# Kernel tuning notes

Hardware: AMD Instinct MI355X
Metric: run time of the kernel (lower is better)

The kernel has to match this reference:

```python
import jax, jax.numpy as jnp
import numpy as np

B, S, N_WIRES, EMBED_DIM, NUM_HEADS = 4, 2048, 8, 512, 8
D_K = EMBED_DIM // NUM_HEADS


def setup_inputs() -> dict:
    key = jax.random.key(0)
    k_x, k_th, k_q, k_k, k_v, k_c = jax.random.split(key, 6)
    x = jax.random.normal(k_x, (B, S, N_WIRES), dtype=jnp.float32)
    # trainable RX rotation angles, one per wire
    theta = jax.random.normal(k_th, (N_WIRES,), dtype=jnp.float32) * 0.1
    # nn.Linear(n_wires, embed_dim, bias=False) weights have shape (embed_dim, n_wires)
    sc_in = 1.0 / np.sqrt(N_WIRES)
    Wq = jax.random.normal(k_q, (EMBED_DIM, N_WIRES), dtype=jnp.float32) * sc_in
    Wk = jax.random.normal(k_k, (EMBED_DIM, N_WIRES), dtype=jnp.float32) * sc_in
    Wv = jax.random.normal(k_v, (EMBED_DIM, N_WIRES), dtype=jnp.float32) * sc_in
    Wc = jax.random.normal(k_c, (EMBED_DIM, EMBED_DIM), dtype=jnp.float32) * (1.0 / np.sqrt(EMBED_DIM))
    return {"x": x, "theta": theta, "Wq": Wq, "Wk": Wk, "Wv": Wv, "Wc": Wc}


def reference(x, theta, Wq, Wk, Wv, Wc):
    # Quantum encoding closed form: RX(x_i) then RX(theta_i) on |0> per wire gives <Z> = cos(x_i + theta_i).
    proj = jnp.cos(x + theta)  # (B, S, n_wires)
    b, s, _ = proj.shape
    q = jnp.einsum('bsn,en->bse', proj, Wq)
    k = jnp.einsum('bsn,en->bse', proj, Wk)
    v = jnp.einsum('bsn,en->bse', proj, Wv)
    # split heads: (B, H, S, d_k)
    q = q.reshape(b, s, NUM_HEADS, D_K).transpose(0, 2, 1, 3)
    k = k.reshape(b, s, NUM_HEADS, D_K).transpose(0, 2, 1, 3)
    v = v.reshape(b, s, NUM_HEADS, D_K).transpose(0, 2, 1, 3)
    scores = jnp.einsum('bhqd,bhkd->bhqk', q, k) / np.sqrt(D_K).astype(np.float32)
    attn = jax.nn.softmax(scores, axis=-1)  # dropout is identity at inference
    out = jnp.einsum('bhqk,bhkd->bhqd', attn, v)
    out = out.transpose(0, 2, 1, 3).reshape(b, s, EMBED_DIM)
    return jnp.einsum('bse,fe->bsf', out, Wc)
```

## Files before the change

### kernel.cpp

```cpp
#include <hip/hip_runtime.h>
#include <stdint.h>

#define N_B 4
#define S_LEN 2048
#define N_H 8
#define E_DIM 512

typedef __attribute__((ext_vector_type(8))) short bf16x8;
typedef __attribute__((ext_vector_type(4))) float f32x4;
typedef __attribute__((ext_vector_type(4))) unsigned int u32x4;
typedef __attribute__((ext_vector_type(2))) unsigned int u32x2;
typedef __attribute__((ext_vector_type(4))) unsigned short u16x4;
typedef __attribute__((ext_vector_type(8))) unsigned short u16x8;

#define MFMA16(a, b, c) __builtin_amdgcn_mfma_f32_16x16x32_bf16((a), (b), (c), 0, 0, 0)

__device__ __forceinline__ unsigned short f2bf(float f) {
    union { float f; unsigned int u; } v; v.f = f;
    unsigned int r = v.u + 0x7fffu + ((v.u >> 16) & 1u);
    return (unsigned short)(r >> 16);
}

__device__ __forceinline__ unsigned int pack2bf(float lo, float hi) {
    union { float f; unsigned int u; } a, b; a.f = lo; b.f = hi;
    return __builtin_amdgcn_perm(b.u + 0x8000u, a.u + 0x8000u, 0x07060302u);
}

__device__ __forceinline__ float fexp2(float x) {
#if __has_builtin(__builtin_amdgcn_exp2f)
    return __builtin_amdgcn_exp2f(x);
#else
    return exp2f(x);
#endif
}

#define Q_SCALE 0.18033688f

__global__ __launch_bounds__(256) void qkv_kernel(
    const float* __restrict__ x, const float* __restrict__ theta,
    const float* __restrict__ Wq, const float* __restrict__ Wk,
    const float* __restrict__ Wv,
    unsigned short* __restrict__ Q, unsigned short* __restrict__ K,
    unsigned short* __restrict__ Vt)
{
    __shared__ float proj[32][8];
    const int tid = threadIdx.x;
    const int mat = blockIdx.x % 3;
    const int chunk = blockIdx.x / 3;
    const int row0 = chunk * 32;
    const int b = row0 >> 11;
    const int s_in_b = row0 & (S_LEN - 1);

    proj[tid >> 3][tid & 7] = cosf(x[row0 * 8 + tid] + theta[tid & 7]);
    __syncthreads();

    if (mat < 2) {
        const float* W = (mat == 0) ? Wq : Wk;
        const float scale = (mat == 0) ? Q_SCALE : 1.0f;
        unsigned short* outp = (mat == 0) ? Q : K;
        const int eg = (tid & 127) * 4;
        const int sg = (tid >> 7) * 16;
        float w[4][8];
        #pragma unroll
        for (int e = 0; e < 4; ++e)
            #pragma unroll
            for (int n = 0; n < 8; ++n)
                w[e][n] = W[(eg + e) * 8 + n] * scale;
        const int h = eg >> 6, d0 = eg & 63;
        unsigned short* p0 = outp + ((size_t)(b * N_H + h) * S_LEN + s_in_b + sg) * 64 + d0;
        #pragma unroll 4
        for (int s = 0; s < 16; ++s) {
            f32x4 pa = *(const f32x4*)&proj[sg + s][0];
            f32x4 pc = *(const f32x4*)&proj[sg + s][4];
            u16x4 o;
            #pragma unroll
            for (int e = 0; e < 4; ++e) {
                float a = 0.f;
                #pragma unroll
                for (int n = 0; n < 4; ++n)
                    a += pa[n] * w[e][n] + pc[n] * w[e][n + 4];
                o[e] = f2bf(a);
            }
            *(u16x4*)&p0[s * 64] = o;
        }
    } else {
        f32x4 ps[8][2];
        const int sl0 = (tid & 3) * 8;
        #pragma unroll
        for (int k2 = 0; k2 < 8; ++k2) {
            ps[k2][0] = *(const f32x4*)&proj[sl0 + k2][0];
            ps[k2][1] = *(const f32x4*)&proj[sl0 + k2][4];
        }
        const int ecol = tid >> 2;
        for (int pass = 0; pass < 8; ++pass) {
            const int e = pass * 64 + ecol;
            const int h = e >> 6, dd = e & 63;
            float wr[8];
            #pragma unroll
            for (int n = 0; n < 8; ++n) wr[n] = Wv[e * 8 + n];
            u16x8 pk;
            #pragma unroll
            for (int k2 = 0; k2 < 8; ++k2) {
                float acc = 0.f;
                #pragma unroll
                for (int n = 0; n < 4; ++n)
                    acc += ps[k2][0][n] * wr[n] + ps[k2][1][n] * wr[n + 4];
                pk[k2] = f2bf(acc);
            }
            *(u16x8*)&Vt[((size_t)(b * N_H + h) * 64 + dd) * S_LEN + s_in_b + sl0] = pk;
        }
    }
}

__global__ __launch_bounds__(256, 4) void flash_kernel(
    const unsigned short* __restrict__ Q, const unsigned short* __restrict__ K,
    const unsigned short* __restrict__ Vt, unsigned short* __restrict__ O)
{
    __shared__ short kt[64 * 72];
    __shared__ short vt[64 * 72];
    __shared__ short pb[128 * 72];

    const int tid = threadIdx.x;
    const int lane = tid & 63, w = tid >> 6;
    const int quad = lane >> 4, lq = lane & 15;
    const int qt = blockIdx.x & 15, bh = blockIdx.x >> 4;
    const int b = bh >> 3, h = bh & 7;

    const unsigned short* Qb = Q + (size_t)bh * S_LEN * 64;
    const unsigned short* Kb = K + (size_t)bh * S_LEN * 64;
    const unsigned short* Vb = Vt + (size_t)bh * 64 * S_LEN;

    bf16x8 qf[2][2];
    #pragma unroll
    for (int mt = 0; mt < 2; ++mt)
        #pragma unroll
        for (int ks = 0; ks < 2; ++ks)
            qf[mt][ks] = *(const bf16x8*)&Qb[(size_t)(qt * 128 + w * 32 + mt * 16 + lq) * 64 + ks * 32 + quad * 8];

    f32x4 oacc[2][4];
    #pragma unroll
    for (int mt = 0; mt < 2; ++mt)
        #pragma unroll
        for (int dt = 0; dt < 4; ++dt) oacc[mt][dt] = 0.f;
    float lsum[2] = {0.f, 0.f};

    u32x4 pkr[2], pvr[2];
    #pragma unroll
    for (int i = 0; i < 2; ++i) {
        const int u = tid + (i << 8);
        pkr[i] = *(const u32x4*)&Kb[(size_t)(u >> 3) * 64 + (u & 7) * 8];
        pvr[i] = *(const u32x4*)&Vb[(size_t)(u >> 3) * S_LEN + (u & 7) * 8];
    }

    for (int kti = 0; kti < 32; ++kti) {
        __syncthreads();
        #pragma unroll
        for (int i = 0; i < 2; ++i) {
            const int u = tid + (i << 8);
            *(u32x4*)&kt[(u >> 3) * 72 + (u & 7) * 8] = pkr[i];
            *(u32x4*)&vt[(u >> 3) * 72 + (u & 7) * 8] = pvr[i];
        }
        __syncthreads();

        const int kb2 = (kti < 31) ? (kti + 1) * 64 : 0;
        #pragma unroll
        for (int i = 0; i < 2; ++i) {
            const int u = tid + (i << 8);
            pkr[i] = *(const u32x4*)&Kb[(size_t)(kb2 + (u >> 3)) * 64 + (u & 7) * 8];
            pvr[i] = *(const u32x4*)&Vb[(size_t)(u >> 3) * S_LEN + kb2 + (u & 7) * 8];
        }

        f32x4 sacc[2][4];
        #pragma unroll
        for (int mt = 0; mt < 2; ++mt)
            #pragma unroll
            for (int mts = 0; mts < 4; ++mts) sacc[mt][mts] = 0.f;
        #pragma unroll
        for (int mts = 0; mts < 4; ++mts) {
            #pragma unroll
            for (int ks = 0; ks < 2; ++ks) {
                bf16x8 af = *(const bf16x8*)&kt[(mts * 16 + lq) * 72 + ks * 32 + quad * 8];
                sacc[0][mts] = MFMA16(af, qf[0][ks], sacc[0][mts]);
                sacc[1][mts] = MFMA16(af, qf[1][ks], sacc[1][mts]);
            }
        }

        #pragma unroll
        for (int mt = 0; mt < 2; ++mt) {
            #pragma unroll
            for (int mts = 0; mts < 4; ++mts) {
                f32x4 p;
                #pragma unroll
                for (int e = 0; e < 4; ++e) p[e] = fexp2(sacc[mt][mts][e]);
                lsum[mt] += (p[0] + p[1]) + (p[2] + p[3]);
                u32x2 pw = { pack2bf(p[0], p[1]), pack2bf(p[2], p[3]) };
                *(u32x2*)&pb[(w * 32 + mt * 16 + lq) * 72 + mts * 16 + quad * 4] = pw;
            }
        }

        #pragma unroll
        for (int ks = 0; ks < 2; ++ks) {
            bf16x8 af0 = *(const bf16x8*)&pb[(w * 32 + lq) * 72 + ks * 32 + quad * 8];
            bf16x8 af1 = *(const bf16x8*)&pb[(w * 32 + 16 + lq) * 72 + ks * 32 + quad * 8];
            #pragma unroll
            for (int dt = 0; dt < 4; ++dt) {
                bf16x8 bf = *(const bf16x8*)&vt[(dt * 16 + lq) * 72 + ks * 32 + quad * 8];
                oacc[0][dt] = MFMA16(af0, bf, oacc[0][dt]);
                oacc[1][dt] = MFMA16(af1, bf, oacc[1][dt]);
            }
        }
    }

    #pragma unroll
    for (int mt = 0; mt < 2; ++mt) {
        float rs = lsum[mt];
        rs += __shfl_xor(rs, 16);
        rs += __shfl_xor(rs, 32);
        const float inv = 1.0f / rs;
        #pragma unroll
        for (int r = 0; r < 4; ++r) {
            const float ir = __shfl(inv, quad * 4 + r);
            const int row = qt * 128 + w * 32 + mt * 16 + quad * 4 + r;
            unsigned short* dst = &O[((size_t)b * S_LEN + row) * E_DIM + h * 64];
            #pragma unroll
            for (int dt = 0; dt < 4; ++dt)
                dst[dt * 16 + lq] = f2bf(oacc[mt][dt][r] * ir);
        }
    }
}

__global__ __launch_bounds__(256, 4) void outproj_kernel(
    const unsigned short* __restrict__ O, const float* __restrict__ Wc,
    float* __restrict__ Y)
{
    __shared__ short at[64 * 72];
    __shared__ short bt[64 * 72];
    const int tid = threadIdx.x;
    const int lane = tid & 63, w = tid >> 6;
    const int quad = lane >> 4, lq = lane & 15;
    const int m0 = (blockIdx.x >> 3) * 64;
    const int f0 = (blockIdx.x & 7) * 64;

    f32x4 acc[4];
    #pragma unroll
    for (int nt = 0; nt < 4; ++nt) acc[nt] = 0.f;

    u32x4 pa[2];
    f32x4 pw[4];
    #pragma unroll
    for (int i = 0; i < 2; ++i) {
        const int u = tid + (i << 8);
        pa[i] = *(const u32x4*)&O[(size_t)(m0 + (u >> 3)) * E_DIM + (u & 7) * 8];
    }
    #pragma unroll
    for (int i = 0; i < 4; ++i) {
        const int u = tid + (i << 8);
        pw[i] = *(const f32x4*)&Wc[(size_t)(f0 + (u >> 4)) * E_DIM + (u & 15) * 4];
    }

    for (int e0 = 0; e0 < E_DIM; e0 += 64) {
        __syncthreads();
        #pragma unroll
        for (int i = 0; i < 2; ++i) {
            const int u = tid + (i << 8);
            *(u32x4*)&at[(u >> 3) * 72 + (u & 7) * 8] = pa[i];
        }
        #pragma unroll
        for (int i = 0; i < 4; ++i) {
            const int u = tid + (i << 8);
            u16x4 pk = { f2bf(pw[i][0]), f2bf(pw[i][1]), f2bf(pw[i][2]), f2bf(pw[i][3]) };
            *(u16x4*)&bt[(u >> 4) * 72 + (u & 15) * 4] = pk;
        }
        __syncthreads();

        const int e1 = (e0 + 64 < E_DIM) ? e0 + 64 : 0;
        #pragma unroll
        for (int i = 0; i < 2; ++i) {
            const int u = tid + (i << 8);
            pa[i] = *(const u32x4*)&O[(size_t)(m0 + (u >> 3)) * E_DIM + e1 + (u & 7) * 8];
        }
        #pragma unroll
        for (int i = 0; i < 4; ++i) {
            const int u = tid + (i << 8);
            pw[i] = *(const f32x4*)&Wc[(size_t)(f0 + (u >> 4)) * E_DIM + e1 + (u & 15) * 4];
        }

        bf16x8 afk[2];
        #pragma unroll
        for (int ks = 0; ks < 2; ++ks)
            afk[ks] = *(const bf16x8*)&at[(w * 16 + lq) * 72 + ks * 32 + quad * 8];
        #pragma unroll
        for (int nt = 0; nt < 4; ++nt) {
            #pragma unroll
            for (int ks = 0; ks < 2; ++ks) {
                bf16x8 bf = *(const bf16x8*)&bt[(nt * 16 + lq) * 72 + ks * 32 + quad * 8];
                acc[nt] = MFMA16(afk[ks], bf, acc[nt]);
            }
        }
    }

    #pragma unroll
    for (int nt = 0; nt < 4; ++nt)
        #pragma unroll
        for (int r = 0; r < 4; ++r)
            Y[(size_t)(m0 + w * 16 + quad * 4 + r) * E_DIM + f0 + nt * 16 + lq] = acc[nt][r];
}

extern "C" void kernel_launch(void* const* d_in, const int* in_sizes, int n_in,
                              void* d_out, int out_size, void* d_ws, size_t ws_size,
                              hipStream_t stream) {
    const float* x     = (const float*)d_in[0];
    const float* theta = (const float*)d_in[1];
    const float* Wq    = (const float*)d_in[2];
    const float* Wk    = (const float*)d_in[3];
    const float* Wv    = (const float*)d_in[4];
    const float* Wc    = (const float*)d_in[5];
    float* Y = (float*)d_out;

    char* ws = (char*)d_ws;
    unsigned short* Q  = (unsigned short*)(ws);
    unsigned short* K  = (unsigned short*)(ws + ((size_t)8 << 20));
    unsigned short* Vt = (unsigned short*)(ws + ((size_t)16 << 20));
    unsigned short* O  = (unsigned short*)(ws + ((size_t)24 << 20));

    qkv_kernel<<<(N_B * S_LEN / 32) * 3, 256, 0, stream>>>(x, theta, Wq, Wk, Wv, Q, K, Vt);
    flash_kernel<<<N_B * N_H * (S_LEN / 128), 256, 0, stream>>>(Q, K, Vt, O);
    outproj_kernel<<<(N_B * S_LEN / 64) * (E_DIM / 64), 256, 0, stream>>>(O, Wc, Y);
}
```

Measured before the change: 142.0 us.

## Split flash attention over two key halves and add a combine kernel

Each flash block now covers half of the key sequence, which doubles the grid from 512 to 1024 blocks to give more parallelism. Partial fp32 outputs and row sums are written to workspace, and a new combine kernel merges them, normalizes and writes bf16 O. V is no longer staged through shared memory; its MFMA operands are read straight from global memory. The change adds extra fp32 partial traffic, an extra launch and uncached strided V loads. Softmax has no running max, so adding the two halves' partial sums stays exact.

```diff
diff --git a/kernel.cpp b/kernel.cpp
--- a/kernel.cpp
+++ b/kernel.cpp
@@ -114,21 +114,22 @@
 
 __global__ __launch_bounds__(256, 4) void flash_kernel(
     const unsigned short* __restrict__ Q, const unsigned short* __restrict__ K,
-    const unsigned short* __restrict__ Vt, unsigned short* __restrict__ O)
+    const unsigned short* __restrict__ Vt,
+    float* __restrict__ OP, float* __restrict__ LS)
 {
     __shared__ short kt[64 * 72];
-    __shared__ short vt[64 * 72];
     __shared__ short pb[128 * 72];
 
     const int tid = threadIdx.x;
     const int lane = tid & 63, w = tid >> 6;
     const int quad = lane >> 4, lq = lane & 15;
-    const int qt = blockIdx.x & 15, bh = blockIdx.x >> 4;
-    const int b = bh >> 3, h = bh & 7;
+    const int kh = blockIdx.x & 1;
+    const int qt = (blockIdx.x >> 1) & 15;
+    const int bh = blockIdx.x >> 5;
 
     const unsigned short* Qb = Q + (size_t)bh * S_LEN * 64;
-    const unsigned short* Kb = K + (size_t)bh * S_LEN * 64;
-    const unsigned short* Vb = Vt + (size_t)bh * 64 * S_LEN;
+    const unsigned short* Kb = K + ((size_t)bh * S_LEN + kh * 1024) * 64;
+    const unsigned short* Vb = Vt + (size_t)bh * 64 * S_LEN + kh * 1024;
 
     bf16x8 qf[2][2];
     #pragma unroll
@@ -144,30 +145,28 @@
         for (int dt = 0; dt < 4; ++dt) oacc[mt][dt] = 0.f;
     float lsum[2] = {0.f, 0.f};
 
-    u32x4 pkr[2], pvr[2];
+    u32x4 pkr[2];
     #pragma unroll
     for (int i = 0; i < 2; ++i) {
         const int u = tid + (i << 8);
         pkr[i] = *(const u32x4*)&Kb[(size_t)(u >> 3) * 64 + (u & 7) * 8];
-        pvr[i] = *(const u32x4*)&Vb[(size_t)(u >> 3) * S_LEN + (u & 7) * 8];
-    }
-
-    for (int kti = 0; kti < 32; ++kti) {
+    }
+
+    for (int kti = 0; kti < 16; ++kti) {
         __syncthreads();
         #pragma unroll
         for (int i = 0; i < 2; ++i) {
             const int u = tid + (i << 8);
             *(u32x4*)&kt[(u >> 3) * 72 + (u & 7) * 8] = pkr[i];
-            *(u32x4*)&vt[(u >> 3) * 72 + (u & 7) * 8] = pvr[i];
         }
         __syncthreads();
 
-        const int kb2 = (kti < 31) ? (kti + 1) * 64 : 0;
+        const int kb = kti * 64;
+        const int kb2 = (kti < 15) ? kb + 64 : 0;
         #pragma unroll
         for (int i = 0; i < 2; ++i) {
             const int u = tid + (i << 8);
             pkr[i] = *(const u32x4*)&Kb[(size_t)(kb2 + (u >> 3)) * 64 + (u & 7) * 8];
-            pvr[i] = *(const u32x4*)&Vb[(size_t)(u >> 3) * S_LEN + kb2 + (u & 7) * 8];
         }
 
         f32x4 sacc[2][4];
@@ -204,28 +203,50 @@
             bf16x8 af1 = *(const bf16x8*)&pb[(w * 32 + 16 + lq) * 72 + ks * 32 + quad * 8];
             #pragma unroll
             for (int dt = 0; dt < 4; ++dt) {
-                bf16x8 bf = *(const bf16x8*)&vt[(dt * 16 + lq) * 72 + ks * 32 + quad * 8];
+                bf16x8 bf = *(const bf16x8*)&Vb[(size_t)(dt * 16 + lq) * S_LEN + kb + ks * 32 + quad * 8];
                 oacc[0][dt] = MFMA16(af0, bf, oacc[0][dt]);
                 oacc[1][dt] = MFMA16(af1, bf, oacc[1][dt]);
             }
         }
     }
 
+    float* OPb = OP + ((size_t)(kh * 32 + bh) * S_LEN + qt * 128) * 64;
+    float* LSb = LS + ((size_t)(kh * 32 + bh) * S_LEN + qt * 128);
     #pragma unroll
     for (int mt = 0; mt < 2; ++mt) {
         float rs = lsum[mt];
         rs += __shfl_xor(rs, 16);
         rs += __shfl_xor(rs, 32);
-        const float inv = 1.0f / rs;
-        #pragma unroll
-        for (int r = 0; r < 4; ++r) {
-            const float ir = __shfl(inv, quad * 4 + r);
-            const int row = qt * 128 + w * 32 + mt * 16 + quad * 4 + r;
-            unsigned short* dst = &O[((size_t)b * S_LEN + row) * E_DIM + h * 64];
-            #pragma unroll
-            for (int dt = 0; dt < 4; ++dt)
-                dst[dt * 16 + lq] = f2bf(oacc[mt][dt][r] * ir);
-        }
+        if (quad == 0) LSb[w * 32 + mt * 16 + lq] = rs;
+        #pragma unroll
+        for (int dt = 0; dt < 4; ++dt)
+            #pragma unroll
+            for (int r = 0; r < 4; ++r)
+                OPb[(size_t)(w * 32 + mt * 16 + quad * 4 + r) * 64 + dt * 16 + lq] = oacc[mt][dt][r];
+    }
+}
+
+__global__ __launch_bounds__(256) void combine_kernel(
+    const float* __restrict__ OP, const float* __restrict__ LS,
+    unsigned short* __restrict__ O)
+{
+    const int t = blockIdx.x * 256 + threadIdx.x;
+    const int bhq = t >> 2;
+    const int dg = (t & 3) << 4;
+    const int bh = bhq >> 11, q = bhq & 2047;
+    const int b = bh >> 3, h = bh & 7;
+    const float ls = LS[(size_t)bh * S_LEN + q] + LS[(size_t)(32 + bh) * S_LEN + q];
+    const float inv = 1.0f / ls;
+    const float* p0 = OP + ((size_t)bh * S_LEN + q) * 64 + dg;
+    const float* p1 = OP + ((size_t)(32 + bh) * S_LEN + q) * 64 + dg;
+    unsigned short* dst = O + ((size_t)b * S_LEN + q) * E_DIM + h * 64 + dg;
+    #pragma unroll
+    for (int c = 0; c < 4; ++c) {
+        f32x4 a = *(const f32x4*)&p0[c * 4];
+        f32x4 bb = *(const f32x4*)&p1[c * 4];
+        u16x4 o = { f2bf((a[0] + bb[0]) * inv), f2bf((a[1] + bb[1]) * inv),
+                    f2bf((a[2] + bb[2]) * inv), f2bf((a[3] + bb[3]) * inv) };
+        *(u16x4*)&dst[c * 4] = o;
     }
 }
 
@@ -321,9 +342,12 @@
     unsigned short* Q  = (unsigned short*)(ws);
     unsigned short* K  = (unsigned short*)(ws + ((size_t)8 << 20));
     unsigned short* Vt = (unsigned short*)(ws + ((size_t)16 << 20));
-    unsigned short* O  = (unsigned short*)(ws + ((size_t)24 << 20));
+    float*          OP = (float*)(ws + ((size_t)24 << 20));
+    float*          LS = (float*)(ws + ((size_t)56 << 20));
+    unsigned short* O  = Q;
 
     qkv_kernel<<<(N_B * S_LEN / 32) * 3, 256, 0, stream>>>(x, theta, Wq, Wk, Wv, Q, K, Vt);
-    flash_kernel<<<N_B * N_H * (S_LEN / 128), 256, 0, stream>>>(Q, K, Vt, O);
+    flash_kernel<<<N_B * N_H * (S_LEN / 128) * 2, 256, 0, stream>>>(Q, K, Vt, OP, LS);
+    combine_kernel<<<(N_B * N_H * S_LEN * 4) / 256, 256, 0, stream>>>(OP, LS, O);
     outproj_kernel<<<(N_B * S_LEN / 64) * (E_DIM / 64), 256, 0, stream>>>(O, Wc, Y);
 }
```

After: 169.0 us. 19.0% more time.
